# Kernel optimization log

Measured on AMD Instinct MI355X. Metric: run time of the kernel, lower is better.

Reference implementation:

```python
import jax, jax.numpy as jnp
import numpy as np

B, N, D, P, HMUL, K = 2, 4096, 64, 64, 4, 16
H = D * HMUL  # attn_mlp hidden = 256
EPS = 1e-5


def setup_inputs() -> dict:
    key = jax.random.key(0)
    ks = jax.random.split(key, 18)
    def lin(k, fan_in, shape):
        return (jax.random.normal(k, shape, dtype=jnp.float32) / np.sqrt(fan_in)).astype(jnp.float32)
    return {
        "x": jax.random.normal(ks[0], (B, N, D), dtype=jnp.float32),
        "pos": jax.random.uniform(ks[1], (B, N, 3), dtype=jnp.float32),
        "w_qkv": lin(ks[2], D, (D, 3 * D)), "b_qkv": jnp.zeros((3 * D,), jnp.float32),
        "w_p1": lin(ks[3], 3, (3, P)),     "b_p1": jnp.zeros((P,), jnp.float32),
        "w_p2": lin(ks[4], P, (P, D)),     "b_p2": jnp.zeros((D,), jnp.float32),
        "w_a1": lin(ks[5], D, (D, H)),     "b_a1": jnp.zeros((H,), jnp.float32),
        "w_a2": lin(ks[6], H, (H, D)),     "b_a2": jnp.zeros((D,), jnp.float32),
        "w_fc": lin(ks[7], D, (D, D)),     "b_fc": jnp.zeros((D,), jnp.float32),
        "gamma": jnp.ones((D,), jnp.float32), "beta": jnp.zeros((D,), jnp.float32),
    }


def reference(x, pos, w_qkv, b_qkv, w_p1, b_p1, w_p2, b_p2,
              w_a1, b_a1, w_a2, b_a2, w_fc, b_fc, gamma, beta):
    residual = x
    qkv = x @ w_qkv + b_qkv                      # [B,N,3D]
    q, k, v = jnp.split(qkv, 3, axis=-1)         # each [B,N,D]

    # full O(N^2) pairwise distances for KNN (smallest-k)
    rel = pos[:, :, None, :] - pos[:, None, :, :]       # [B,N,N,3]
    dist = jnp.sqrt(jnp.sum(rel * rel, axis=-1))        # [B,N,N]
    _, idx = jax.lax.top_k(-dist, K)                    # [B,N,K] nearest indices

    # gather neighbors (gather commutes with the pointwise MLPs the torch
    # code applies before its neighbor_select, so math is identical)
    gather = jax.vmap(lambda arr, i: arr[i])            # arr:[N,*], i:[N,K] -> [N,K,*]
    k_nb = gather(k, idx)                               # [B,N,K,D]
    v_nb = gather(v, idx)                               # [B,N,K,D]
    pos_nb = gather(pos, idx)                           # [B,N,K,3]

    qk_map = q[:, :, None, :] - k_nb                    # [B,N,K,D]
    rel_nb = pos[:, :, None, :] - pos_nb                # [B,N,K,3]
    pos_emb = jax.nn.relu(rel_nb @ w_p1 + b_p1) @ w_p2 + b_p2   # [B,N,K,D]

    h = qk_map + pos_emb
    scores = jax.nn.relu(h @ w_a1 + b_a1) @ w_a2 + b_a2          # [B,N,K,D]
    attn = jax.nn.softmax(scores, axis=-2)                       # over K neighbors
    agg = jnp.sum(attn * v_nb, axis=-2)                          # [B,N,D]

    agg = agg @ w_fc + b_fc
    # BatchNorm1d over channel dim D (training-mode batch stats over B and N)
    mean = jnp.mean(agg, axis=(0, 1))
    var = jnp.mean(jnp.square(agg - mean), axis=(0, 1))
    agg = (agg - mean) * jax.lax.rsqrt(var + EPS) * gamma + beta
    return jax.nn.relu(agg) + residual
```

## Files before the change

### kernel.cpp

```cpp
#include <hip/hip_runtime.h>
#include <hip/hip_bf16.h>
#include <math.h>

#define NPTS 4096
#define KNB 16
#define CAP 384
#define QPB 8

typedef __attribute__((ext_vector_type(8))) short bf16x8;
typedef __attribute__((ext_vector_type(4))) float f32x4;
#define MFMA16(a, b, c) __builtin_amdgcn_mfma_f32_16x16x32_bf16(a, b, c, 0, 0, 0)

__device__ __forceinline__ unsigned short f2bf(float f) {
  unsigned int u = __float_as_uint(f);
  unsigned int r = (u + 0x7fffu + ((u >> 16) & 1u)) >> 16;
  return (unsigned short)r;
}

__global__ __launch_bounds__(256) void qkv_pack_kernel(
    const float* __restrict__ x, const float* __restrict__ w_qkv,
    const float* __restrict__ b_qkv, float* __restrict__ qkv,
    const float* __restrict__ w_a1, const float* __restrict__ w_a2,
    const float* __restrict__ w_p2, unsigned short* __restrict__ pk1,
    unsigned short* __restrict__ pk2, unsigned short* __restrict__ pkp,
    float* __restrict__ stats) {
  int tid = threadIdx.x, bid = blockIdx.x;

  if (bid == 272) {
    if (tid < 128) stats[tid] = 0.f;
    return;
  }
  if (bid >= 128) {
    int e = (bid - 128) * 256 + tid;
    if (e < 16384) {
      int j = e & 7, lane = (e >> 3) & 63, t = e >> 9;
      int ks = t & 1, nt = t >> 1;
      int k = ks * 32 + ((lane >> 4) << 3) + j, n = nt * 16 + (lane & 15);
      pk1[e] = f2bf(w_a1[k * 256 + n]);
    } else if (e < 32768) {
      int e2 = e - 16384;
      int j = e2 & 7, lane = (e2 >> 3) & 63, t = e2 >> 9;
      int ks = t & 7, nt = t >> 3;
      int k = ks * 32 + ((lane >> 4) << 3) + j, n = nt * 16 + (lane & 15);
      pk2[e2] = f2bf(w_a2[k * 64 + n]);
    } else if (e < 36864) {
      int e3 = e - 32768;
      int j = e3 & 7, lane = (e3 >> 3) & 63, t = e3 >> 9;
      int ks = t & 1, nt = t >> 1;
      int k = ks * 32 + ((lane >> 4) << 3) + j, n = nt * 16 + (lane & 15);
      pkp[e3] = f2bf(w_p2[k * 64 + n]);
    }
    return;
  }

  int lane = tid & 63, w = tid >> 6;
  int m = lane & 15, quad = lane >> 4;
  int r0w = bid * 64 + w * 16;

  const float* xr = x + (size_t)(r0w + m) * 64;
  float xa[8], xb[8];
  *(float4*)&xa[0] = *(const float4*)(xr + quad * 8);
  *(float4*)&xa[4] = *(const float4*)(xr + quad * 8 + 4);
  *(float4*)&xb[0] = *(const float4*)(xr + 32 + quad * 8);
  *(float4*)&xb[4] = *(const float4*)(xr + 32 + quad * 8 + 4);
  bf16x8 a0, a1;
#pragma unroll
  for (int j = 0; j < 8; ++j) {
    a0[j] = (short)f2bf(xa[j]);
    a1[j] = (short)f2bf(xb[j]);
  }

#pragma unroll 4
  for (int nt = 0; nt < 12; ++nt) {
    int n = nt * 16 + m;
    int k0 = quad * 8;
    bf16x8 b0, b1;
#pragma unroll
    for (int j = 0; j < 8; ++j) {
      b0[j] = (short)f2bf(w_qkv[(size_t)(k0 + j) * 192 + n]);
      b1[j] = (short)f2bf(w_qkv[(size_t)(32 + k0 + j) * 192 + n]);
    }
    f32x4 acc = {0.f, 0.f, 0.f, 0.f};
    acc = MFMA16(a0, b0, acc);
    acc = MFMA16(a1, b1, acc);
    float bb = b_qkv[n];
#pragma unroll
    for (int i = 0; i < 4; ++i)
      qkv[(size_t)(r0w + quad * 4 + i) * 192 + n] = acc[i] + bb;
  }
}

__global__ __launch_bounds__(256, 4) void fused_kernel(
    const float* __restrict__ qkv, const float* __restrict__ pos,
    const unsigned short* __restrict__ pk1,
    const unsigned short* __restrict__ pk2,
    const unsigned short* __restrict__ pkp, const float* __restrict__ w_p1,
    const float* __restrict__ b_p1, const float* __restrict__ b_p2,
    const float* __restrict__ b_a1, const float* __restrict__ b_a2,
    const float* __restrict__ w_fc, const float* __restrict__ b_fc,
    float* __restrict__ y, float* __restrict__ stats) {
  __shared__ __align__(16) char smem[25216];
  __shared__ int s_idx[128];

  int tid = threadIdx.x, lane = tid & 63, w = tid >> 6;
  int m = lane & 15, quad = lane >> 4;
  int g0 = blockIdx.x * QPB;
  int b = g0 >> 12;
  const float* posb = pos + (size_t)b * NPTS * 3;

  {
    unsigned int(*cbits)[CAP] = (unsigned int(*)[CAP])smem;
    int(*cidx)[CAP] = (int(*)[CAP])(smem + 12288);
    unsigned long long* wmin = (unsigned long long*)(smem + 24576);
    float* sretry = (float*)(smem + 24608);
    unsigned int* scnt = (unsigned int*)(smem + 24640);
    unsigned long long* sprev = (unsigned long long*)(smem + 24672);
    int* sany = (int*)(smem + 24680);

    float qx[QPB], qy[QPB], qz[QPB], t2q[QPB];
#pragma unroll
    for (int q = 0; q < QPB; ++q) {
      int i = (g0 + q) & (NPTS - 1);
      qx[q] = posb[i * 3 + 0];
      qy[q] = posb[i * 3 + 1];
      qz[q] = posb[i * 3 + 2];
    }
#pragma unroll
    for (int q = 0; q < QPB; ++q) {
      float r = 0.141f;
#pragma unroll
      for (int it = 0; it < 3; ++it) {
        float inv2r = 0.5f / r;
        float fx = (fminf(qx[q] + r, 1.f) - fmaxf(qx[q] - r, 0.f)) * inv2r;
        float fy = (fminf(qy[q] + r, 1.f) - fmaxf(qy[q] - r, 0.f)) * inv2r;
        float fz = (fminf(qz[q] + r, 1.f) - fmaxf(qz[q] - r, 0.f)) * inv2r;
        float expn = 17157.28f * r * r * r * fx * fy * fz;
        float s = exp2f(0.33333334f * log2f(48.f / expn));
        s = fminf(fmaxf(s, 0.7f), 1.6f);
        r = fminf(r * s, 0.32f);
      }
      t2q[q] = r * r;
    }
    if (tid < QPB) scnt[tid] = 0;
    if (tid == 0) sany[0] = 0;
    __syncthreads();

    for (int c = 0; c < NPTS / 256; ++c) {
      int j = c * 256 + tid;
      int j3 = j * 3;
      float px = posb[j3 + 0], py = posb[j3 + 1], pz = posb[j3 + 2];
#pragma unroll
      for (int q = 0; q < QPB; ++q) {
        float dx = qx[q] - px, dy = qy[q] - py, dz = qz[q] - pz;
        float d2 = fmaf(dz, dz, fmaf(dy, dy, dx * dx));
        bool hit = d2 < t2q[q];
        unsigned long long mask = __ballot(hit);
        if (mask) {
          if (hit) {
            unsigned int p = atomicAdd(&scnt[q], 1u);
            if (p < CAP) {
              cbits[q][p] = __float_as_uint(d2);
              cidx[q][p] = j;
            }
          }
        }
      }
    }
    __syncthreads();

    if (tid < QPB) {
      int q = tid;
      unsigned int n = scnt[q];
      float nt = 0.f;
      if (n < KNB) nt = t2q[q] * 4.f;
      else if (n > CAP) nt = t2q[q] * 0.4f;
      sretry[q] = nt;
      if (nt != 0.f) {
        scnt[q] = 0;
        sany[0] = 1;
      }
    }
    __syncthreads();

    if (sany[0]) {
      float tr[QPB];
#pragma unroll
      for (int q = 0; q < QPB; ++q) tr[q] = sretry[q];
      for (int c = 0; c < NPTS / 256; ++c) {
        int j = c * 256 + tid;
        int j3 = j * 3;
        float px = posb[j3 + 0], py = posb[j3 + 1], pz = posb[j3 + 2];
#pragma unroll
        for (int q = 0; q < QPB; ++q) {
          if (tr[q] != 0.f) {
            float dx = qx[q] - px, dy = qy[q] - py, dz = qz[q] - pz;
            float d2 = fmaf(dz, dz, fmaf(dy, dy, dx * dx));
            bool hit = d2 < tr[q];
            unsigned long long mask = __ballot(hit);
            if (mask) {
              if (hit) {
                unsigned int p = atomicAdd(&scnt[q], 1u);
                if (p < CAP) {
                  cbits[q][p] = __float_as_uint(d2);
                  cidx[q][p] = j;
                }
              }
            }
          }
        }
      }
      __syncthreads();
    }

    for (int qq = 0; qq < 2; ++qq) {
      int q = w * 2 + qq;
      int L = (int)scnt[q];
      if (L >= KNB && L <= CAP) {
        for (int i = lane; i < L; i += 64) {
          unsigned long long ki = ((unsigned long long)cbits[q][i] << 32) |
                                  (unsigned int)cidx[q][i];
          int rank = 0;
          for (int mm = 0; mm < L; ++mm) {
            unsigned long long km = ((unsigned long long)cbits[q][mm] << 32) |
                                    (unsigned int)cidx[q][mm];
            rank += km < ki;
          }
          if (rank < KNB) s_idx[q * KNB + rank] = cidx[q][i];
        }
      }
    }
    __syncthreads();

    for (int q = 0; q < QPB; ++q) {
      unsigned int n = scnt[q];
      if (n < KNB || n > CAP) {
        unsigned long long prev = 0ull;
        for (int r = 0; r < KNB; ++r) {
          unsigned long long best = ~0ull;
          for (int c = 0; c < NPTS / 256; ++c) {
            int j = c * 256 + tid;
            float dx = qx[q] - posb[j * 3 + 0];
            float dy = qy[q] - posb[j * 3 + 1];
            float dz = qz[q] - posb[j * 3 + 2];
            float d2 = fmaf(dz, dz, fmaf(dy, dy, dx * dx));
            unsigned long long key =
                ((unsigned long long)__float_as_uint(d2) << 32) |
                (unsigned int)j;
            bool ok = (r == 0) || (key > prev);
            best = (ok && key < best) ? key : best;
          }
#pragma unroll
          for (int off = 32; off > 0; off >>= 1) {
            unsigned long long o = __shfl_down(best, off);
            best = best < o ? best : o;
          }
          if (lane == 0) wmin[w] = best;
          __syncthreads();
          if (tid == 0) {
            unsigned long long m0 = wmin[0], m1 = wmin[1];
            unsigned long long m2 = wmin[2], m3 = wmin[3];
            unsigned long long a = m0 < m1 ? m0 : m1;
            unsigned long long d = m2 < m3 ? m2 : m3;
            a = a < d ? a : d;
            s_idx[q * KNB + r] = (int)(unsigned int)a;
            sprev[0] = a;
          }
          __syncthreads();
          prev = sprev[0];
          __syncthreads();
        }
      }
    }
  }
  __syncthreads();

  unsigned short(*region)[72] = (unsigned short(*)[72])smem;
  float(*s_rel)[32][3] = (float(*)[32][3])(smem + 18432);

  if (lane < 32) {
    int row = 32 * w + lane;
    int p = lane >> 4;
    int g = g0 + 2 * w + p;
    int jb = (b << 12) | s_idx[row];
    s_rel[w][lane][0] = pos[(size_t)g * 3 + 0] - pos[(size_t)jb * 3 + 0];
    s_rel[w][lane][1] = pos[(size_t)g * 3 + 1] - pos[(size_t)jb * 3 + 1];
    s_rel[w][lane][2] = pos[(size_t)g * 3 + 2] - pos[(size_t)jb * 3 + 2];
  }

  {
    float w0 = w_p1[lane], w1 = w_p1[64 + lane], w2 = w_p1[128 + lane];
    float bp = b_p1[lane];
    for (int rl = 0; rl < 32; ++rl) {
      int row = 32 * w + rl;
      float rx = s_rel[w][rl][0], ry = s_rel[w][rl][1], rz = s_rel[w][rl][2];
      float e = fmaf(rz, w2, fmaf(ry, w1, fmaf(rx, w0, bp)));
      region[row][lane] = f2bf(fmaxf(e, 0.f));
    }
  }

  {
    bf16x8 ea0[2], ea1[2];
#pragma unroll
    for (int p = 0; p < 2; ++p) {
      ea0[p] = *(const bf16x8*)&region[32 * w + 16 * p + m][quad * 8];
      ea1[p] = *(const bf16x8*)&region[32 * w + 16 * p + m][32 + quad * 8];
    }
#pragma unroll
    for (int nt = 0; nt < 4; ++nt) {
      bf16x8 b0 = *(const bf16x8*)(pkp + ((size_t)(nt * 2 + 0) * 64 + lane) * 8);
      bf16x8 b1 = *(const bf16x8*)(pkp + ((size_t)(nt * 2 + 1) * 64 + lane) * 8);
      int col = nt * 16 + m;
      float bp2 = b_p2[col];
#pragma unroll
      for (int p = 0; p < 2; ++p) {
        f32x4 acc = {0.f, 0.f, 0.f, 0.f};
        acc = MFMA16(ea0[p], b0, acc);
        acc = MFMA16(ea1[p], b1, acc);
        int g = g0 + 2 * w + p;
        float qv = qkv[(size_t)g * 192 + col];
#pragma unroll
        for (int i = 0; i < 4; ++i) {
          int row = 32 * w + 16 * p + quad * 4 + i;
          int jb = (b << 12) | s_idx[row];
          float kv = qkv[(size_t)jb * 192 + 64 + col];
          region[row][col] = f2bf(qv - kv + acc[i] + bp2);
        }
      }
    }
  }

  float vreg[2][4][4];
#pragma unroll
  for (int p = 0; p < 2; ++p)
#pragma unroll
    for (int i = 0; i < 4; ++i) {
      int row = 32 * w + 16 * p + quad * 4 + i;
      int jb = (b << 12) | s_idx[row];
      const float* vr = qkv + (size_t)jb * 192 + 128;
#pragma unroll
      for (int nt2 = 0; nt2 < 4; ++nt2) vreg[p][nt2][i] = vr[nt2 * 16 + m];
    }

  bf16x8 ha0[2], ha1[2];
#pragma unroll
  for (int p = 0; p < 2; ++p) {
    ha0[p] = *(const bf16x8*)&region[32 * w + 16 * p + m][quad * 8];
    ha1[p] = *(const bf16x8*)&region[32 * w + 16 * p + m][32 + quad * 8];
  }
  f32x4 acc2[2][4];
#pragma unroll
  for (int p = 0; p < 2; ++p)
#pragma unroll
    for (int nt2 = 0; nt2 < 4; ++nt2) acc2[p][nt2] = (f32x4){0.f, 0.f, 0.f, 0.f};

  unsigned short(*s_tc)[72] = (unsigned short(*)[72])(smem + w * 4608);

#pragma unroll
  for (int c = 0; c < 4; ++c) {
#pragma unroll
    for (int ntc = 0; ntc < 4; ++ntc) {
      int nt = 4 * c + ntc;
      bf16x8 b0 = *(const bf16x8*)(pk1 + ((size_t)(nt * 2 + 0) * 64 + lane) * 8);
      bf16x8 b1 = *(const bf16x8*)(pk1 + ((size_t)(nt * 2 + 1) * 64 + lane) * 8);
      int coll = ntc * 16 + m;
      float ba = b_a1[nt * 16 + m];
#pragma unroll
      for (int p = 0; p < 2; ++p) {
        f32x4 t = {0.f, 0.f, 0.f, 0.f};
        t = MFMA16(ha0[p], b0, t);
        t = MFMA16(ha1[p], b1, t);
#pragma unroll
        for (int i = 0; i < 4; ++i)
          s_tc[16 * p + quad * 4 + i][coll] = f2bf(fmaxf(t[i] + ba, 0.f));
      }
    }
#pragma unroll
    for (int sub = 0; sub < 2; ++sub) {
      int ks = c * 2 + sub;
      bf16x8 a[2];
#pragma unroll
      for (int p = 0; p < 2; ++p)
        a[p] = *(const bf16x8*)&s_tc[16 * p + m][sub * 32 + quad * 8];
#pragma unroll
      for (int nt2 = 0; nt2 < 4; ++nt2) {
        bf16x8 bb =
            *(const bf16x8*)(pk2 + ((size_t)(nt2 * 8 + ks) * 64 + lane) * 8);
#pragma unroll
        for (int p = 0; p < 2; ++p) acc2[p][nt2] = MFMA16(a[p], bb, acc2[p][nt2]);
      }
    }
  }

  float ba2[4];
#pragma unroll
  for (int nt2 = 0; nt2 < 4; ++nt2) ba2[nt2] = b_a2[nt2 * 16 + m];
  float aggv[2][4];
#pragma unroll
  for (int p = 0; p < 2; ++p) {
#pragma unroll
    for (int nt2 = 0; nt2 < 4; ++nt2) {
      float sc[4];
#pragma unroll
      for (int i = 0; i < 4; ++i) sc[i] = acc2[p][nt2][i] + ba2[nt2];
      float mx = fmaxf(fmaxf(sc[0], sc[1]), fmaxf(sc[2], sc[3]));
      mx = fmaxf(mx, __shfl_xor(mx, 16));
      mx = fmaxf(mx, __shfl_xor(mx, 32));
      float ex[4], ss = 0.f;
#pragma unroll
      for (int i = 0; i < 4; ++i) {
        ex[i] = exp2f((sc[i] - mx) * 1.4426950408889634f);
        ss += ex[i];
      }
      ss += __shfl_xor(ss, 16);
      ss += __shfl_xor(ss, 32);
      float nu = 0.f;
#pragma unroll
      for (int i = 0; i < 4; ++i) nu = fmaf(ex[i], vreg[p][nt2][i], nu);
      nu += __shfl_xor(nu, 16);
      nu += __shfl_xor(nu, 32);
      aggv[p][nt2] = nu / ss;
    }
  }
  __syncthreads();

  float* s_agg = (float*)smem;
  if (quad == 0) {
#pragma unroll
    for (int p = 0; p < 2; ++p)
#pragma unroll
      for (int nt2 = 0; nt2 < 4; ++nt2)
        s_agg[(2 * w + p) * 64 + nt2 * 16 + m] = aggv[p][nt2];
  }
  __syncthreads();

  {
    int c = lane, r = w;
    float acc0 = b_fc[c], acc1 = b_fc[c];
    for (int d = 0; d < 64; ++d) {
      float wv = w_fc[d * 64 + c];
      acc0 = fmaf(s_agg[r * 64 + d], wv, acc0);
      acc1 = fmaf(s_agg[(r + 4) * 64 + d], wv, acc1);
    }
    y[(size_t)(g0 + r) * 64 + c] = acc0;
    y[(size_t)(g0 + r + 4) * 64 + c] = acc1;
    float* s_red = (float*)(smem + 2048);
    float* s_red2 = (float*)(smem + 3072);
    s_red[w * 64 + c] = acc0 + acc1;
    s_red2[w * 64 + c] = acc0 * acc0 + acc1 * acc1;
  }
  __syncthreads();
  if (tid < 64) {
    float* s_red = (float*)(smem + 2048);
    float* s_red2 = (float*)(smem + 3072);
    float s = s_red[tid] + s_red[64 + tid] + s_red[128 + tid] + s_red[192 + tid];
    float s2 =
        s_red2[tid] + s_red2[64 + tid] + s_red2[128 + tid] + s_red2[192 + tid];
    atomicAdd(&stats[tid], s);
    atomicAdd(&stats[64 + tid], s2);
  }
}

__global__ __launch_bounds__(256) void bn_kernel(
    const float* __restrict__ y, const float* __restrict__ x,
    const float* __restrict__ stats, const float* __restrict__ gamma,
    const float* __restrict__ beta, float* __restrict__ out) {
  size_t o = (size_t)blockIdx.x * 256 + threadIdx.x;
  int c = (int)(o & 63);
  const float inv_n = 1.f / 8192.f;
  float mean = stats[c] * inv_n;
  float var = stats[64 + c] * inv_n - mean * mean;
  float inv = rsqrtf(var + 1e-5f);
  float v = (y[o] - mean) * inv * gamma[c] + beta[c];
  out[o] = fmaxf(v, 0.f) + x[o];
}

extern "C" void kernel_launch(void* const* d_in, const int* in_sizes, int n_in,
                              void* d_out, int out_size, void* d_ws,
                              size_t ws_size, hipStream_t stream) {
  const float* x = (const float*)d_in[0];
  const float* pos = (const float*)d_in[1];
  const float* w_qkv = (const float*)d_in[2];
  const float* b_qkv = (const float*)d_in[3];
  const float* w_p1 = (const float*)d_in[4];
  const float* b_p1 = (const float*)d_in[5];
  const float* w_p2 = (const float*)d_in[6];
  const float* b_p2 = (const float*)d_in[7];
  const float* w_a1 = (const float*)d_in[8];
  const float* b_a1 = (const float*)d_in[9];
  const float* w_a2 = (const float*)d_in[10];
  const float* b_a2 = (const float*)d_in[11];
  const float* w_fc = (const float*)d_in[12];
  const float* b_fc = (const float*)d_in[13];
  const float* gamma = (const float*)d_in[14];
  const float* beta = (const float*)d_in[15];

  char* ws = (char*)d_ws;
  float* qkv = (float*)(ws + 0);
  float* y = (float*)(ws + 8912896);
  float* stats = (float*)(ws + 11010048);
  unsigned short* pk1 = (unsigned short*)(ws + 11010560);
  unsigned short* pk2 = (unsigned short*)(ws + 11043328);
  unsigned short* pkp = (unsigned short*)(ws + 11076096);

  hipLaunchKernelGGL(qkv_pack_kernel, dim3(273), dim3(256), 0, stream, x,
                     w_qkv, b_qkv, qkv, w_a1, w_a2, w_p2, pk1, pk2, pkp,
                     stats);
  hipLaunchKernelGGL(fused_kernel, dim3(1024), dim3(256), 0, stream, qkv, pos,
                     pk1, pk2, pkp, w_p1, b_p1, b_p2, b_a1, b_a2, w_fc, b_fc,
                     y, stats);
  hipLaunchKernelGGL(bn_kernel, dim3(2048), dim3(256), 0, stream, y, x, stats,
                     gamma, beta, (float*)d_out);
}
```

Measured before the change: 150.9 us.

## Pre-pack QKV weights in separate kernel and shrink KNN search radius

Splits the combined kernel into a weight-packing kernel and a QKV projection kernel. The projection now reads pre-packed bf16 MFMA fragments for w_qkv instead of gathering and converting strided fp32 weights in every block, and uses 16-row blocks with each wave handling 3 column tiles, giving 512 blocks. It also lowers the initial KNN candidate radius and the target expected neighbour count (48 to 38), which shrinks the candidate set to reduce filtering work. The trade-offs are an extra kernel launch and a higher chance of retry passes when fewer than 16 candidates fall inside the radius.

```diff
diff --git a/kernel.cpp b/kernel.cpp
--- a/kernel.cpp
+++ b/kernel.cpp
@@ -17,47 +17,48 @@
   return (unsigned short)r;
 }
 
-__global__ __launch_bounds__(256) void qkv_pack_kernel(
-    const float* __restrict__ x, const float* __restrict__ w_qkv,
-    const float* __restrict__ b_qkv, float* __restrict__ qkv,
-    const float* __restrict__ w_a1, const float* __restrict__ w_a2,
-    const float* __restrict__ w_p2, unsigned short* __restrict__ pk1,
+__global__ __launch_bounds__(256) void pack_kernel(
+    const float* __restrict__ w_qkv, const float* __restrict__ w_a1,
+    const float* __restrict__ w_a2, const float* __restrict__ w_p2,
+    unsigned short* __restrict__ pkq, unsigned short* __restrict__ pk1,
     unsigned short* __restrict__ pk2, unsigned short* __restrict__ pkp,
     float* __restrict__ stats) {
-  int tid = threadIdx.x, bid = blockIdx.x;
-
-  if (bid == 272) {
-    if (tid < 128) stats[tid] = 0.f;
-    return;
-  }
-  if (bid >= 128) {
-    int e = (bid - 128) * 256 + tid;
-    if (e < 16384) {
-      int j = e & 7, lane = (e >> 3) & 63, t = e >> 9;
-      int ks = t & 1, nt = t >> 1;
-      int k = ks * 32 + ((lane >> 4) << 3) + j, n = nt * 16 + (lane & 15);
-      pk1[e] = f2bf(w_a1[k * 256 + n]);
-    } else if (e < 32768) {
-      int e2 = e - 16384;
-      int j = e2 & 7, lane = (e2 >> 3) & 63, t = e2 >> 9;
-      int ks = t & 7, nt = t >> 3;
-      int k = ks * 32 + ((lane >> 4) << 3) + j, n = nt * 16 + (lane & 15);
-      pk2[e2] = f2bf(w_a2[k * 64 + n]);
-    } else if (e < 36864) {
-      int e3 = e - 32768;
-      int j = e3 & 7, lane = (e3 >> 3) & 63, t = e3 >> 9;
-      int ks = t & 1, nt = t >> 1;
-      int k = ks * 32 + ((lane >> 4) << 3) + j, n = nt * 16 + (lane & 15);
-      pkp[e3] = f2bf(w_p2[k * 64 + n]);
-    }
-    return;
-  }
-
-  int lane = tid & 63, w = tid >> 6;
+  int e = blockIdx.x * 256 + threadIdx.x;
+  if (e < 128) stats[e] = 0.f;
+  if (e < 12288) {
+    int j = e & 7, lane = (e >> 3) & 63, t = e >> 9;
+    int ks = t & 1, nt = t >> 1;
+    int k = ks * 32 + ((lane >> 4) << 3) + j, n = nt * 16 + (lane & 15);
+    pkq[e] = f2bf(w_qkv[k * 192 + n]);
+  } else if (e < 28672) {
+    int e1 = e - 12288;
+    int j = e1 & 7, lane = (e1 >> 3) & 63, t = e1 >> 9;
+    int ks = t & 1, nt = t >> 1;
+    int k = ks * 32 + ((lane >> 4) << 3) + j, n = nt * 16 + (lane & 15);
+    pk1[e1] = f2bf(w_a1[k * 256 + n]);
+  } else if (e < 45056) {
+    int e2 = e - 28672;
+    int j = e2 & 7, lane = (e2 >> 3) & 63, t = e2 >> 9;
+    int ks = t & 7, nt = t >> 3;
+    int k = ks * 32 + ((lane >> 4) << 3) + j, n = nt * 16 + (lane & 15);
+    pk2[e2] = f2bf(w_a2[k * 64 + n]);
+  } else if (e < 49152) {
+    int e3 = e - 45056;
+    int j = e3 & 7, lane = (e3 >> 3) & 63, t = e3 >> 9;
+    int ks = t & 1, nt = t >> 1;
+    int k = ks * 32 + ((lane >> 4) << 3) + j, n = nt * 16 + (lane & 15);
+    pkp[e3] = f2bf(w_p2[k * 64 + n]);
+  }
+}
+
+__global__ __launch_bounds__(256) void qkv_kernel(
+    const float* __restrict__ x, const unsigned short* __restrict__ pkq,
+    const float* __restrict__ b_qkv, float* __restrict__ qkv) {
+  int tid = threadIdx.x, lane = tid & 63, w = tid >> 6;
   int m = lane & 15, quad = lane >> 4;
-  int r0w = bid * 64 + w * 16;
-
-  const float* xr = x + (size_t)(r0w + m) * 64;
+  int r0 = blockIdx.x * 16;
+
+  const float* xr = x + (size_t)(r0 + m) * 64;
   float xa[8], xb[8];
   *(float4*)&xa[0] = *(const float4*)(xr + quad * 8);
   *(float4*)&xa[4] = *(const float4*)(xr + quad * 8 + 4);
@@ -70,23 +71,19 @@
     a1[j] = (short)f2bf(xb[j]);
   }
 
-#pragma unroll 4
-  for (int nt = 0; nt < 12; ++nt) {
+#pragma unroll
+  for (int t = 0; t < 3; ++t) {
+    int nt = w * 3 + t;
+    bf16x8 b0 = *(const bf16x8*)(pkq + ((size_t)(nt * 2 + 0) * 64 + lane) * 8);
+    bf16x8 b1 = *(const bf16x8*)(pkq + ((size_t)(nt * 2 + 1) * 64 + lane) * 8);
     int n = nt * 16 + m;
-    int k0 = quad * 8;
-    bf16x8 b0, b1;
-#pragma unroll
-    for (int j = 0; j < 8; ++j) {
-      b0[j] = (short)f2bf(w_qkv[(size_t)(k0 + j) * 192 + n]);
-      b1[j] = (short)f2bf(w_qkv[(size_t)(32 + k0 + j) * 192 + n]);
-    }
     f32x4 acc = {0.f, 0.f, 0.f, 0.f};
     acc = MFMA16(a0, b0, acc);
     acc = MFMA16(a1, b1, acc);
     float bb = b_qkv[n];
 #pragma unroll
     for (int i = 0; i < 4; ++i)
-      qkv[(size_t)(r0w + quad * 4 + i) * 192 + n] = acc[i] + bb;
+      qkv[(size_t)(r0 + quad * 4 + i) * 192 + n] = acc[i] + bb;
   }
 }
 
@@ -127,7 +124,7 @@
     }
 #pragma unroll
     for (int q = 0; q < QPB; ++q) {
-      float r = 0.141f;
+      float r = 0.131f;
 #pragma unroll
       for (int it = 0; it < 3; ++it) {
         float inv2r = 0.5f / r;
@@ -135,7 +132,7 @@
         float fy = (fminf(qy[q] + r, 1.f) - fmaxf(qy[q] - r, 0.f)) * inv2r;
         float fz = (fminf(qz[q] + r, 1.f) - fmaxf(qz[q] - r, 0.f)) * inv2r;
         float expn = 17157.28f * r * r * r * fx * fy * fz;
-        float s = exp2f(0.33333334f * log2f(48.f / expn));
+        float s = exp2f(0.33333334f * log2f(38.f / expn));
         s = fminf(fmaxf(s, 0.7f), 1.6f);
         r = fminf(r * s, 0.32f);
       }
@@ -501,10 +498,12 @@
   unsigned short* pk1 = (unsigned short*)(ws + 11010560);
   unsigned short* pk2 = (unsigned short*)(ws + 11043328);
   unsigned short* pkp = (unsigned short*)(ws + 11076096);
-
-  hipLaunchKernelGGL(qkv_pack_kernel, dim3(273), dim3(256), 0, stream, x,
-                     w_qkv, b_qkv, qkv, w_a1, w_a2, w_p2, pk1, pk2, pkp,
-                     stats);
+  unsigned short* pkq = (unsigned short*)(ws + 11084288);
+
+  hipLaunchKernelGGL(pack_kernel, dim3(192), dim3(256), 0, stream, w_qkv,
+                     w_a1, w_a2, w_p2, pkq, pk1, pk2, pkp, stats);
+  hipLaunchKernelGGL(qkv_kernel, dim3(512), dim3(256), 0, stream, x, pkq,
+                     b_qkv, qkv);
   hipLaunchKernelGGL(fused_kernel, dim3(1024), dim3(256), 0, stream, qkv, pos,
                      pk1, pk2, pkp, w_p1, b_p1, b_p2, b_a1, b_a2, w_fc, b_fc,
                      y, stats);
```

Result: no change. 150.6 us (-0.2%).
